# Optimization experiments

Measured on AMD Instinct MI355X. Metric: run time of the kernel, lower is better.

Reference implementation:

```python
import jax, jax.numpy as jnp
import numpy as np

N_NODES = 50000
N_EDGES = 800000
DIMX = 64
DIMY = 32
NSMAT = 64
N_MID = 6  # six hidden nsmat->nsmat layers between the input and output projections


def setup_inputs() -> dict:
    key = jax.random.key(0)
    ks = jax.random.split(key, 10)
    node_features = jax.random.normal(ks[0], (N_NODES, DIMX), dtype=jnp.float32)
    edge_index = jax.random.randint(ks[1], (2, N_EDGES), 0, N_NODES, dtype=jnp.int64)
    s_in = 1.0 / np.sqrt(DIMX)
    s_mid = 1.0 / np.sqrt(NSMAT)
    w_in = jax.random.uniform(ks[2], (DIMX, NSMAT), jnp.float32, -s_in, s_in)
    b_in = jax.random.uniform(ks[3], (NSMAT,), jnp.float32, -s_in, s_in)
    w_mid = jax.random.uniform(ks[4], (N_MID, NSMAT, NSMAT), jnp.float32, -s_mid, s_mid)
    b_mid = jax.random.uniform(ks[5], (N_MID, NSMAT), jnp.float32, -s_mid, s_mid)
    w_out = jax.random.uniform(ks[6], (NSMAT, DIMY * DIMX), jnp.float32, -s_mid, s_mid)
    b_out = jax.random.uniform(ks[7], (DIMY * DIMX,), jnp.float32, -s_mid, s_mid)
    return {"node_features": node_features, "edge_index": edge_index,
            "w_in": w_in, "b_in": b_in, "w_mid": w_mid, "b_mid": b_mid,
            "w_out": w_out, "b_out": b_out}


def reference(node_features, edge_index, w_in, b_in, w_mid, b_mid, w_out, b_out):
    # per-node MLP producing a [dimy, dimx] sheaf matrix
    h = jax.nn.relu(node_features @ w_in + b_in)
    for i in range(N_MID):  # fixed small layer count
        h = jax.nn.relu(h @ w_mid[i] + b_mid[i])
    smat = (h @ w_out + b_out).reshape(-1, DIMY, DIMX)  # [N, dimy, dimx]
    # batched matrix-vector transform: q_n = smat_n @ x_n
    q = jnp.einsum('nyx,nx->ny', smat, node_features)  # [N, dimy]
    # LightGCN conv: out_i = sum_{(j->i) in E} q_j / sqrt(deg_j * deg_i)
    row, col = edge_index[0], edge_index[1]
    deg = jax.ops.segment_sum(jnp.ones((N_EDGES,), q.dtype), col, num_segments=N_NODES)
    dinv = jnp.where(deg > 0, jax.lax.rsqrt(jnp.maximum(deg, 1.0)), 0.0)
    norm = dinv[row] * dinv[col]  # [E]
    out = jax.ops.segment_sum(norm[:, None] * q[row], col, num_segments=N_NODES)
    return out
```

## Files before the change

kernel.cpp:

```cpp
#include <hip/hip_runtime.h>
#include <cstddef>

#define N_NODES_C 50000
#define N_NODES_PAD 50048
#define N_EDGES_C 800000

typedef _Float16 f16x8 __attribute__((ext_vector_type(8)));
typedef float    f32x4 __attribute__((ext_vector_type(4)));

constexpr int XSTR = 72;
constexpr int MQ_BLOCKS   = 782;
constexpr int FILL_BLOCKS = 782;
constexpr int DEG_BLOCKS  = 782;

__device__ __forceinline__ void gll16(const void* g, void* l) {
    __builtin_amdgcn_global_load_lds(
        (const __attribute__((address_space(1))) void*)g,
        (__attribute__((address_space(3))) void*)l, 16, 0, 0);
}

__global__ void prep_deg_kernel(const float* __restrict__ w_in,
                                const float* __restrict__ w_mid,
                                const float* __restrict__ w_out,
                                const int* __restrict__ col,
                                _Float16* __restrict__ wT,
                                _Float16* __restrict__ W3T,
                                int* __restrict__ deg4,
                                int* __restrict__ rank)
{
    const int b = blockIdx.x;
    if (b < 624) {
        const int idx = b * 256 + threadIdx.x;
        if (idx < 7 * 4096) {
            const int l = idx >> 12, rem = idx & 4095;
            const int k = rem >> 6, j = rem & 63;
            const float v = (l == 0) ? w_in[k * 64 + j]
                                     : w_mid[(size_t)(l - 1) * 4096 + k * 64 + j];
            wT[(size_t)l * 4096 + j * 64 + k] = (_Float16)v;
        } else {
            const int i2 = idx - 7 * 4096;
            const int k = i2 >> 11, r = i2 & 2047;
            const int c = k >> 3;
            const int pos = ((c ^ (r & 7)) << 3) | (k & 7);
            W3T[(size_t)r * 64 + pos] = (_Float16)w_out[(size_t)k * 2048 + r];
        }
    } else {
        const int e0 = (b - 624) * 1024 + threadIdx.x;
        #pragma unroll
        for (int k = 0; k < 4; ++k) {
            const int e = e0 + k * 256;
            if (e < N_EDGES_C)
                rank[e] = atomicAdd(&deg4[k * N_NODES_C + col[e]], 1);
        }
    }
}

__global__ void scan1_kernel(const int* __restrict__ deg4, int* __restrict__ bsum)
{
    const int t = threadIdx.x;
    const int i = blockIdx.x * 256 + t;
    int v = 0;
    if (i < N_NODES_C) {
        #pragma unroll
        for (int k = 0; k < 4; ++k) v += deg4[k * N_NODES_C + i];
    }
    #pragma unroll
    for (int d = 1; d < 64; d <<= 1) v += __shfl_xor(v, d);
    __shared__ int s[4];
    if ((t & 63) == 0) s[t >> 6] = v;
    __syncthreads();
    if (t == 0) bsum[blockIdx.x] = s[0] + s[1] + s[2] + s[3];
}

__global__ void scan2_kernel(const int* __restrict__ bsum, int* __restrict__ boff,
                             int* __restrict__ rowptr)
{
    __shared__ int sh[256];
    const int t = threadIdx.x;
    const int v = (t < 196) ? bsum[t] : 0;
    sh[t] = v;
    __syncthreads();
    for (int d = 1; d < 256; d <<= 1) {
        const int u = (t >= d) ? sh[t - d] : 0;
        __syncthreads();
        sh[t] += u;
        __syncthreads();
    }
    if (t < 196) boff[t] = sh[t] - v;
    if (t == 0) rowptr[N_NODES_C] = N_EDGES_C;
}

__global__ void scan3_kernel(const int* __restrict__ deg4, const int* __restrict__ boff,
                             int* __restrict__ rowptr, int* __restrict__ shoff,
                             float* __restrict__ dinv)
{
    const int t = threadIdx.x;
    const int i = blockIdx.x * 256 + t;
    const int lane = t & 63, w = t >> 6;
    int d[4];
    int v = 0;
    if (i < N_NODES_C) {
        #pragma unroll
        for (int k = 0; k < 4; ++k) { d[k] = deg4[k * N_NODES_C + i]; v += d[k]; }
    } else {
        d[0] = d[1] = d[2] = d[3] = 0;
    }
    int inc = v;
    #pragma unroll
    for (int dd = 1; dd < 64; dd <<= 1) {
        const int u = __shfl_up(inc, dd);
        if (lane >= dd) inc += u;
    }
    __shared__ int ws[4];
    if (lane == 63) ws[w] = inc;
    __syncthreads();
    int wo = 0;
    #pragma unroll
    for (int k = 0; k < 4; ++k) if (k < w) wo += ws[k];
    const int excl = boff[blockIdx.x] + wo + inc - v;
    if (i < N_NODES_C) {
        rowptr[i] = excl;
        dinv[i] = (v > 0) ? rsqrtf((float)v) : 0.f;
        int o = excl;
        shoff[0 * N_NODES_C + i] = o; o += d[0];
        shoff[1 * N_NODES_C + i] = o; o += d[1];
        shoff[2 * N_NODES_C + i] = o; o += d[2];
        shoff[3 * N_NODES_C + i] = o;
    }
}

__launch_bounds__(256, 4)
__global__ void mega_kernel(const float* __restrict__ xf,
                            const float* __restrict__ b_in,
                            const float* __restrict__ b_mid,
                            const _Float16* __restrict__ wT,
                            const _Float16* __restrict__ W3T,
                            const float* __restrict__ b_out,
                            const float* __restrict__ dinv,
                            float* __restrict__ qs,
                            const int* __restrict__ row,
                            const int* __restrict__ col,
                            const int* __restrict__ shoff,
                            const int* __restrict__ rank,
                            int* __restrict__ src)
{
    __shared__ _Float16 smem[16896];

    if (blockIdx.x >= MQ_BLOCKS) {
        const int base = (blockIdx.x - MQ_BLOCKS) * 1024 + threadIdx.x;
        #pragma unroll
        for (int u = 0; u < 4; ++u) {
            const int e = base + u * 256;
            if (e < N_EDGES_C) {
                const int c = col[e];
                const int kk = (e >> 8) & 3;
                const int slot = shoff[kk * N_NODES_C + c] + rank[e];
                src[slot] = row[e];
            }
        }
        return;
    }

    const int t    = threadIdx.x;
    const int w    = t >> 6;
    const int lane = t & 63;
    const int quad = lane >> 4;
    const int lrow = lane & 15;
    const int node0 = blockIdx.x * 64 + w * 16;
    _Float16* hb = &smem[w * 16 * XSTR];

    {
        const int n = min(node0 + lrow, N_NODES_C - 1);
        const float4* src4 = (const float4*)(xf + (size_t)n * 64 + quad * 16);
        _Float16 tmp[16];
        #pragma unroll
        for (int i = 0; i < 4; ++i) {
            const float4 v = src4[i];
            tmp[i * 4 + 0] = (_Float16)v.x;
            tmp[i * 4 + 1] = (_Float16)v.y;
            tmp[i * 4 + 2] = (_Float16)v.z;
            tmp[i * 4 + 3] = (_Float16)v.w;
        }
        *(f16x8*)&hb[lrow * XSTR + quad * 16]     = *(f16x8*)&tmp[0];
        *(f16x8*)&hb[lrow * XSTR + quad * 16 + 8] = *(f16x8*)&tmp[8];
    }

    {
        const _Float16* wTl = wT;
        const float* bsrc = b_in;
        for (int l = 0; l < 7; ++l) {
            const f16x8 A0 = *(const f16x8*)&hb[lrow * XSTR + quad * 8];
            const f16x8 A1 = *(const f16x8*)&hb[lrow * XSTR + 32 + quad * 8];
            #pragma unroll
            for (int Nt = 0; Nt < 4; ++Nt) {
                const f16x8 B0 = *(const f16x8*)(wTl + (Nt * 16 + lrow) * 64 + quad * 8);
                const f16x8 B1 = *(const f16x8*)(wTl + (Nt * 16 + lrow) * 64 + 32 + quad * 8);
                const float bias = bsrc[Nt * 16 + lrow];
                f32x4 C = {0.f, 0.f, 0.f, 0.f};
                C = __builtin_amdgcn_mfma_f32_16x16x32_f16(A0, B0, C, 0, 0, 0);
                C = __builtin_amdgcn_mfma_f32_16x16x32_f16(A1, B1, C, 0, 0, 0);
                #pragma unroll
                for (int r = 0; r < 4; ++r) {
                    const float v = fmaxf(C[r] + bias, 0.f);
                    hb[(quad * 4 + r) * XSTR + Nt * 16 + lrow] = (_Float16)v;
                }
            }
            wTl += 4096;
            bsrc = b_mid + (size_t)l * 64;
        }
    }

    const int ra = node0 + lrow;
    const int na = min(ra, N_NODES_C - 1);

    f16x8 Bha[2];
    #pragma unroll
    for (int ks = 0; ks < 2; ++ks)
        Bha[ks] = *(const f16x8*)&hb[lrow * XSTR + ks * 32 + quad * 8];
    float4 xca[4];
    #pragma unroll
    for (int xt = 0; xt < 4; ++xt)
        xca[xt] = *(const float4*)(xf + (size_t)na * 64 + xt * 16 + quad * 4);
    const float dva = dinv[na];

    __syncthreads();

    {
        float* lb = (float*)smem;
        const float* gb = b_out + (size_t)(w * 64 + lane) * 4;
        gll16(gb,        lb + w * 256);
        gll16(gb + 1024, lb + 1024 + w * 256);
        #pragma unroll
        for (int s = 0; s < 2; ++s) {
            _Float16* ld = &smem[4608 + s * 4096 + w * 512];
            const _Float16* gs = W3T + (size_t)s * 4096 + (size_t)(w * 64 + lane) * 8;
            gll16(gs,        ld);
            gll16(gs + 2048, ld + 2048);
        }
    }

    const int swz = lrow & 7;
    const int cp0 = ((quad)     ^ swz) * 8;
    const int cp1 = ((4 + quad) ^ swz) * 8;
    const float* lbf = (const float*)smem;

    int rcur = 0;
    for (int y = 0; y < 32; ++y) {
        if (y == 0)      asm volatile("s_waitcnt vmcnt(2)" ::: "memory");
        else if (y == 1) asm volatile("s_waitcnt vmcnt(3)" ::: "memory");
        else             asm volatile("s_waitcnt vmcnt(4)" ::: "memory");
        __builtin_amdgcn_s_barrier();
        __builtin_amdgcn_sched_barrier(0);

        {
            const int ys = (y + 2) & 31;
            const int ri = (rcur == 0) ? 2 : rcur - 1;
            _Float16* ld = &smem[4608 + ri * 4096 + w * 512];
            const _Float16* gs = W3T + (size_t)ys * 4096 + (size_t)(w * 64 + lane) * 8;
            gll16(gs,        ld);
            gll16(gs + 2048, ld + 2048);
        }

        const _Float16* cur = &smem[4608 + rcur * 4096];
        float qa = 0.f;
        #pragma unroll
        for (int xt = 0; xt < 4; ++xt) {
            const _Float16* rp = cur + (xt * 16 + lrow) * 64;
            const f16x8 A0 = *(const f16x8*)(rp + cp0);
            const f16x8 A1 = *(const f16x8*)(rp + cp1);
            f32x4 Ca = {0.f, 0.f, 0.f, 0.f};
            Ca = __builtin_amdgcn_mfma_f32_16x16x32_f16(A0, Bha[0], Ca, 0, 0, 0);
            Ca = __builtin_amdgcn_mfma_f32_16x16x32_f16(A1, Bha[1], Ca, 0, 0, 0);

            const float4 bf = *(const float4*)(lbf + y * 64 + xt * 16 + quad * 4);
            qa += (Ca[0] + bf.x) * xca[xt].x + (Ca[1] + bf.y) * xca[xt].y
                + (Ca[2] + bf.z) * xca[xt].z + (Ca[3] + bf.w) * xca[xt].w;
        }
        qa += __shfl_xor(qa, 16);
        qa += __shfl_xor(qa, 32);

        if (quad == (y >> 3)) {
            qs[(size_t)ra * 32 + y] = qa * dva;
        }

        rcur = (rcur == 2) ? 0 : rcur + 1;
    }
}

__global__ void gather_kernel(const int* __restrict__ rowptr, const int* __restrict__ src,
                              const float* __restrict__ qs, const float* __restrict__ dinv,
                              float* __restrict__ out)
{
    const int t = threadIdx.x;
    const int node = blockIdx.x * 32 + (t >> 3);
    if (node >= N_NODES_C) return;
    const int yq = (t & 7) * 4;
    const int s0 = rowptr[node];
    const int s1 = rowptr[node + 1];
    float4 acc = {0.f, 0.f, 0.f, 0.f};
    int s = s0;
    for (; s + 4 <= s1; s += 4) {
        const int r0 = src[s], r1 = src[s + 1], r2 = src[s + 2], r3 = src[s + 3];
        const float4 a0 = *(const float4*)(qs + (size_t)r0 * 32 + yq);
        const float4 a1 = *(const float4*)(qs + (size_t)r1 * 32 + yq);
        const float4 a2 = *(const float4*)(qs + (size_t)r2 * 32 + yq);
        const float4 a3 = *(const float4*)(qs + (size_t)r3 * 32 + yq);
        acc.x += a0.x + a1.x + a2.x + a3.x;
        acc.y += a0.y + a1.y + a2.y + a3.y;
        acc.z += a0.z + a1.z + a2.z + a3.z;
        acc.w += a0.w + a1.w + a2.w + a3.w;
    }
    for (; s < s1; ++s) {
        const float4 a = *(const float4*)(qs + (size_t)src[s] * 32 + yq);
        acc.x += a.x; acc.y += a.y; acc.z += a.z; acc.w += a.w;
    }
    const float dv = dinv[node];
    float4 r;
    r.x = acc.x * dv; r.y = acc.y * dv; r.z = acc.z * dv; r.w = acc.w * dv;
    *(float4*)(out + (size_t)node * 32 + yq) = r;
}

extern "C" void kernel_launch(void* const* d_in, const int* in_sizes, int n_in,
                              void* d_out, int out_size, void* d_ws, size_t ws_size,
                              hipStream_t stream)
{
    const float* xf    = (const float*)d_in[0];
    const int*   eidx  = (const int*)d_in[1];
    const float* w_in  = (const float*)d_in[2];
    const float* b_in  = (const float*)d_in[3];
    const float* w_mid = (const float*)d_in[4];
    const float* b_mid = (const float*)d_in[5];
    const float* w_out = (const float*)d_in[6];
    const float* b_out = (const float*)d_in[7];
    float* out = (float*)d_out;

    const int* row = eidx;
    const int* col = eidx + N_EDGES_C;

    char* ws = (char*)d_ws;
    float*    qs     = (float*)(ws + 0);
    int*      deg4   = (int*)(ws + 6406144);
    float*    dinv   = (float*)(ws + 7206144);
    _Float16* wT     = (_Float16*)(ws + 7406144);
    _Float16* W3T    = (_Float16*)(ws + 7463488);
    int*      rowptr = (int*)(ws + 7725632);
    int*      shoff  = (int*)(ws + 7925636);
    int*      rank   = (int*)(ws + 8725636);
    int*      srcb   = (int*)(ws + 11925636);
    int*      bsum   = (int*)(ws + 15125636);
    int*      boff   = (int*)(ws + 15126420);

    hipMemsetAsync(deg4, 0, 4 * N_NODES_C * sizeof(int), stream);

    prep_deg_kernel<<<dim3(624 + DEG_BLOCKS), dim3(256), 0, stream>>>(
        w_in, w_mid, w_out, col, wT, W3T, deg4, rank);

    scan1_kernel<<<dim3(196), dim3(256), 0, stream>>>(deg4, bsum);
    scan2_kernel<<<dim3(1), dim3(256), 0, stream>>>(bsum, boff, rowptr);
    scan3_kernel<<<dim3(196), dim3(256), 0, stream>>>(deg4, boff, rowptr, shoff, dinv);

    mega_kernel<<<dim3(MQ_BLOCKS + FILL_BLOCKS), dim3(256), 0, stream>>>(
        xf, b_in, b_mid, wT, W3T, b_out, dinv, qs, row, col, shoff, rank, srcb);

    gather_kernel<<<dim3(1563), dim3(256), 0, stream>>>(rowptr, srcb, qs, dinv, out);
}
```

Baseline: 189.9 us.

## Split output-projection y-rows across waves with per-wave W3 ring buffers

Each wave now handles all 64 nodes of the block for a strided subset of output rows y, keeping the hidden activations for four 16-node groups in registers. The W3 slices are streamed into private per-wave double-buffered LDS rings, so the per-row block barrier is gone. The goal is to cut redundant W3 LDS traffic and the block-wide synchronization in the y loop. In exchange, LDS use and register pressure rise a lot, so the launch bound drops to two blocks per CU and occupancy falls.

```diff
diff --git a/kernel.cpp b/kernel.cpp
--- a/kernel.cpp
+++ b/kernel.cpp
@@ -129,7 +129,7 @@
     }
 }
 
-__launch_bounds__(256, 4)
+__launch_bounds__(256, 2)
 __global__ void mega_kernel(const float* __restrict__ xf,
                             const float* __restrict__ b_in,
                             const float* __restrict__ b_mid,
@@ -144,7 +144,7 @@
                             const int* __restrict__ rank,
                             int* __restrict__ src)
 {
-    __shared__ _Float16 smem[16896];
+    __shared__ _Float16 smem[37376];
 
     if (blockIdx.x >= MQ_BLOCKS) {
         const int base = (blockIdx.x - MQ_BLOCKS) * 1024 + threadIdx.x;
@@ -210,18 +210,25 @@
         }
     }
 
-    const int ra = node0 + lrow;
-    const int na = min(ra, N_NODES_C - 1);
-
-    f16x8 Bha[2];
-    #pragma unroll
-    for (int ks = 0; ks < 2; ++ks)
-        Bha[ks] = *(const f16x8*)&hb[lrow * XSTR + ks * 32 + quad * 8];
-    float4 xca[4];
-    #pragma unroll
-    for (int xt = 0; xt < 4; ++xt)
-        xca[xt] = *(const float4*)(xf + (size_t)na * 64 + xt * 16 + quad * 4);
-    const float dva = dinv[na];
+    __syncthreads();
+
+    f16x8 Bh[4][2];
+    #pragma unroll
+    for (int g = 0; g < 4; ++g)
+        #pragma unroll
+        for (int ks = 0; ks < 2; ++ks)
+            Bh[g][ks] = *(const f16x8*)&smem[g * 16 * XSTR + lrow * XSTR + ks * 32 + quad * 8];
+
+    float4 xc[4][4];
+    #pragma unroll
+    for (int g = 0; g < 4; ++g) {
+        const int na = min(blockIdx.x * 64 + g * 16 + lrow, N_NODES_C - 1);
+        #pragma unroll
+        for (int xt = 0; xt < 4; ++xt)
+            xc[g][xt] = *(const float4*)(xf + (size_t)na * 64 + xt * 16 + quad * 4);
+    }
+    const int nself = blockIdx.x * 64 + lane;
+    const float dsel = dinv[min(nself, N_NODES_C - 1)];
 
     __syncthreads();
 
@@ -230,60 +237,84 @@
         const float* gb = b_out + (size_t)(w * 64 + lane) * 4;
         gll16(gb,        lb + w * 256);
         gll16(gb + 1024, lb + 1024 + w * 256);
+        __builtin_amdgcn_sched_barrier(0);
+        _Float16* ring = &smem[4608 + w * 8192];
         #pragma unroll
         for (int s = 0; s < 2; ++s) {
-            _Float16* ld = &smem[4608 + s * 4096 + w * 512];
-            const _Float16* gs = W3T + (size_t)s * 4096 + (size_t)(w * 64 + lane) * 8;
-            gll16(gs,        ld);
-            gll16(gs + 2048, ld + 2048);
-        }
-    }
+            const int y = s * 4 + w;
+            #pragma unroll
+            for (int g8 = 0; g8 < 8; ++g8)
+                gll16(W3T + (size_t)y * 4096 + g8 * 512 + (size_t)lane * 8,
+                      ring + s * 4096 + g8 * 512);
+        }
+        __builtin_amdgcn_sched_barrier(0);
+    }
+    asm volatile("s_waitcnt vmcnt(16)" ::: "memory");
+    __builtin_amdgcn_s_barrier();
+    __builtin_amdgcn_sched_barrier(0);
 
     const int swz = lrow & 7;
     const int cp0 = ((quad)     ^ swz) * 8;
     const int cp1 = ((4 + quad) ^ swz) * 8;
     const float* lbf = (const float*)smem;
-
-    int rcur = 0;
-    for (int y = 0; y < 32; ++y) {
-        if (y == 0)      asm volatile("s_waitcnt vmcnt(2)" ::: "memory");
-        else if (y == 1) asm volatile("s_waitcnt vmcnt(3)" ::: "memory");
-        else             asm volatile("s_waitcnt vmcnt(4)" ::: "memory");
-        __builtin_amdgcn_s_barrier();
-        __builtin_amdgcn_sched_barrier(0);
-
-        {
-            const int ys = (y + 2) & 31;
-            const int ri = (rcur == 0) ? 2 : rcur - 1;
-            _Float16* ld = &smem[4608 + ri * 4096 + w * 512];
-            const _Float16* gs = W3T + (size_t)ys * 4096 + (size_t)(w * 64 + lane) * 8;
-            gll16(gs,        ld);
-            gll16(gs + 2048, ld + 2048);
-        }
-
-        const _Float16* cur = &smem[4608 + rcur * 4096];
-        float qa = 0.f;
+    _Float16* ring = &smem[4608 + w * 8192];
+
+    #pragma unroll
+    for (int yy = 0; yy < 8; ++yy) {
+        if (yy == 0)      asm volatile("s_waitcnt vmcnt(8)" ::: "memory");
+        else if (yy == 7) asm volatile("s_waitcnt vmcnt(1)" ::: "memory");
+        else              asm volatile("s_waitcnt vmcnt(9)" ::: "memory");
+        __builtin_amdgcn_sched_barrier(0);
+
+        const int y = yy * 4 + w;
+        const _Float16* cur = ring + (yy & 1) * 4096;
+        float q0 = 0.f, q1 = 0.f, q2 = 0.f, q3 = 0.f;
         #pragma unroll
         for (int xt = 0; xt < 4; ++xt) {
             const _Float16* rp = cur + (xt * 16 + lrow) * 64;
             const f16x8 A0 = *(const f16x8*)(rp + cp0);
             const f16x8 A1 = *(const f16x8*)(rp + cp1);
-            f32x4 Ca = {0.f, 0.f, 0.f, 0.f};
-            Ca = __builtin_amdgcn_mfma_f32_16x16x32_f16(A0, Bha[0], Ca, 0, 0, 0);
-            Ca = __builtin_amdgcn_mfma_f32_16x16x32_f16(A1, Bha[1], Ca, 0, 0, 0);
+            f32x4 C0 = {0.f,0.f,0.f,0.f}, C1 = {0.f,0.f,0.f,0.f};
+            f32x4 C2 = {0.f,0.f,0.f,0.f}, C3 = {0.f,0.f,0.f,0.f};
+            C0 = __builtin_amdgcn_mfma_f32_16x16x32_f16(A0, Bh[0][0], C0, 0, 0, 0);
+            C0 = __builtin_amdgcn_mfma_f32_16x16x32_f16(A1, Bh[0][1], C0, 0, 0, 0);
+            C1 = __builtin_amdgcn_mfma_f32_16x16x32_f16(A0, Bh[1][0], C1, 0, 0, 0);
+            C1 = __builtin_amdgcn_mfma_f32_16x16x32_f16(A1, Bh[1][1], C1, 0, 0, 0);
+            C2 = __builtin_amdgcn_mfma_f32_16x16x32_f16(A0, Bh[2][0], C2, 0, 0, 0);
+            C2 = __builtin_amdgcn_mfma_f32_16x16x32_f16(A1, Bh[2][1], C2, 0, 0, 0);
+            C3 = __builtin_amdgcn_mfma_f32_16x16x32_f16(A0, Bh[3][0], C3, 0, 0, 0);
+            C3 = __builtin_amdgcn_mfma_f32_16x16x32_f16(A1, Bh[3][1], C3, 0, 0, 0);
 
             const float4 bf = *(const float4*)(lbf + y * 64 + xt * 16 + quad * 4);
-            qa += (Ca[0] + bf.x) * xca[xt].x + (Ca[1] + bf.y) * xca[xt].y
-                + (Ca[2] + bf.z) * xca[xt].z + (Ca[3] + bf.w) * xca[xt].w;
-        }
-        qa += __shfl_xor(qa, 16);
-        qa += __shfl_xor(qa, 32);
-
-        if (quad == (y >> 3)) {
-            qs[(size_t)ra * 32 + y] = qa * dva;
-        }
-
-        rcur = (rcur == 2) ? 0 : rcur + 1;
+            q0 += (C0[0] + bf.x) * xc[0][xt].x + (C0[1] + bf.y) * xc[0][xt].y
+                + (C0[2] + bf.z) * xc[0][xt].z + (C0[3] + bf.w) * xc[0][xt].w;
+            q1 += (C1[0] + bf.x) * xc[1][xt].x + (C1[1] + bf.y) * xc[1][xt].y
+                + (C1[2] + bf.z) * xc[1][xt].z + (C1[3] + bf.w) * xc[1][xt].w;
+            q2 += (C2[0] + bf.x) * xc[2][xt].x + (C2[1] + bf.y) * xc[2][xt].y
+                + (C2[2] + bf.z) * xc[2][xt].z + (C2[3] + bf.w) * xc[2][xt].w;
+            q3 += (C3[0] + bf.x) * xc[3][xt].x + (C3[1] + bf.y) * xc[3][xt].y
+                + (C3[2] + bf.z) * xc[3][xt].z + (C3[3] + bf.w) * xc[3][xt].w;
+        }
+        q0 += __shfl_xor(q0, 16); q0 += __shfl_xor(q0, 32);
+        q1 += __shfl_xor(q1, 16); q1 += __shfl_xor(q1, 32);
+        q2 += __shfl_xor(q2, 16); q2 += __shfl_xor(q2, 32);
+        q3 += __shfl_xor(q3, 16); q3 += __shfl_xor(q3, 32);
+
+        const float qv = (quad == 0) ? q0 : (quad == 1) ? q1 : (quad == 2) ? q2 : q3;
+        qs[(size_t)nself * 32 + y] = qv * dsel;
+
+        __builtin_amdgcn_sched_barrier(0);
+        if (yy + 2 < 8) {
+            const int yn = (yy + 2) * 4 + w;
+            _Float16* dst = ring + (yy & 1) * 4096;
+            asm volatile("s_waitcnt lgkmcnt(0)" ::: "memory");
+            __builtin_amdgcn_sched_barrier(0);
+            #pragma unroll
+            for (int g8 = 0; g8 < 8; ++g8)
+                gll16(W3T + (size_t)yn * 4096 + g8 * 512 + (size_t)lane * 8,
+                      dst + g8 * 512);
+        }
+        __builtin_amdgcn_sched_barrier(0);
     }
 }
 
```

After: 192.0 us. No clear change (+1.1%).
